# Kernel optimization log

Hardware: AMD Instinct MI355X
Metric: run time of the kernel (lower is better)

The kernel has to match this reference:

```python
import jax, jax.numpy as jnp
import numpy as np

B, D, E, H = 4, 128, 512, 512

def setup_inputs() -> dict:
    key = jax.random.key(0)
    k1, k2, k3, k4, k5 = jax.random.split(key, 5)
    s = 1.0 / np.sqrt(H)
    return {
        "x_decoder": jax.random.normal(k1, (B, D, H), dtype=jnp.float32),
        "x_encoder": jax.random.normal(k2, (B, E, H), dtype=jnp.float32),
        "mask": jnp.zeros((B, E), dtype=bool),
        "W1": jax.random.uniform(k3, (H, H), jnp.float32, -s, s),  # nn.Linear weight (out,in)
        "W2": jax.random.uniform(k4, (H, H), jnp.float32, -s, s),
        "v": jax.random.uniform(k5, (H,), jnp.float32, -s, s),     # Linear(H,1) weight squeezed
    }

def reference(x_decoder, x_encoder, mask, W1, W2, v):
    # w1(x_encoder): (B,E,H); w2(x_decoder): (B,D,H)
    enc_t = jnp.einsum('beh,oh->beo', x_encoder, W1)
    dec_t = jnp.einsum('bdh,oh->bdo', x_decoder, W2)
    # additive attention: tanh over broadcast sum (B,D,E,H), reduce with v -> (B,D,E)
    prod = jnp.einsum('bdeh,h->bde', jnp.tanh(dec_t[:, :, None, :] + enc_t[:, None, :, :]), v)
    prod = jnp.where(mask[:, None, :], -jnp.inf, prod)
    return jax.nn.log_softmax(prod, axis=-1)
```

## Files before the change

### kernel.cpp

```cpp
#include <hip/hip_runtime.h>
#include <math.h>

#define BATCH 4
#define DDIM  128
#define EDIM  512
#define HDIM  512

#define TANH_SCALE 2.8853900817779268f

typedef short short8v __attribute__((ext_vector_type(8)));
typedef float f32x4   __attribute__((ext_vector_type(4)));

#define EXP2F(x) __builtin_amdgcn_exp2f(x)
#define RCPF(x)  __builtin_amdgcn_rcpf(x)

static __device__ inline unsigned short f2bf(float f) {
    unsigned u = __float_as_uint(f);
    return (unsigned short)((u + 0x7FFFu + ((u >> 16) & 1u)) >> 16);
}
static __device__ inline unsigned pack_bf2(float f0, float f1) {
    unsigned u0 = __float_as_uint(f0), u1 = __float_as_uint(f1);
    u0 += 0x7FFFu + ((u0 >> 16) & 1u);
    u1 += 0x7FFFu + ((u1 >> 16) & 1u);
    return __builtin_amdgcn_perm(u1, u0, 0x07060302u);
}
static __device__ inline float bf2f(unsigned short h) {
    return __uint_as_float(((unsigned)h) << 16);
}

__global__ __launch_bounds__(256)
void gemm_both(const float* __restrict__ xdec, const float* __restrict__ W2,
               const float* __restrict__ xenc, const float* __restrict__ W1,
               unsigned short* __restrict__ P, unsigned short* __restrict__ Q) {
    __shared__ unsigned short As[2][64][40];
    __shared__ unsigned short Bs[2][64][40];

    const int id = blockIdx.x;
    const float *Ab, *Bb;
    unsigned short* Cb;
    int m0, n0;
    if (id < 64) {
        int b = id >> 4, r = id & 15;
        m0 = (r >> 3) * 64; n0 = (r & 7) * 64;
        Ab = xdec + (long)b * DDIM * HDIM;
        Bb = W2;
        Cb = P + (long)b * DDIM * HDIM;
    } else {
        int t2 = id - 64;
        int b = t2 >> 6, r = t2 & 63;
        m0 = (r >> 3) * 64; n0 = (r & 7) * 64;
        Ab = W1;
        Bb = xenc + (long)b * EDIM * HDIM;
        Cb = Q + (long)b * HDIM * EDIM;
    }

    const int t    = threadIdx.x;
    const int srow = t >> 2;
    const int skq  = (t & 3) << 3;

    const int wid = t >> 6, wm = wid >> 1, wn = wid & 1;
    const int l   = t & 63, lr = l & 15, c16 = l >> 4;

    f32x4 acc[2][2] = {};

    const float* ap = Ab + (long)(m0 + srow) * HDIM + skq;
    const float* bp = Bb + (long)(n0 + srow) * HDIM + skq;

    float4 a0 = *(const float4*)ap, a1 = *(const float4*)(ap + 4);
    float4 b0 = *(const float4*)bp, b1 = *(const float4*)(bp + 4);

    int cur = 0;
    for (int k0 = 0; k0 < HDIM; k0 += 32) {
        uint4 apk, bpk;
        apk.x = pack_bf2(a0.x, a0.y); apk.y = pack_bf2(a0.z, a0.w);
        apk.z = pack_bf2(a1.x, a1.y); apk.w = pack_bf2(a1.z, a1.w);
        bpk.x = pack_bf2(b0.x, b0.y); bpk.y = pack_bf2(b0.z, b0.w);
        bpk.z = pack_bf2(b1.x, b1.y); bpk.w = pack_bf2(b1.z, b1.w);
        *(uint4*)&As[cur][srow][skq] = apk;
        *(uint4*)&Bs[cur][srow][skq] = bpk;

        if (k0 + 32 < HDIM) {
            ap += 32; bp += 32;
            a0 = *(const float4*)ap; a1 = *(const float4*)(ap + 4);
            b0 = *(const float4*)bp; b1 = *(const float4*)(bp + 4);
        }

        asm volatile("s_waitcnt lgkmcnt(0)" ::: "memory");
        __builtin_amdgcn_s_barrier();
        __builtin_amdgcn_sched_barrier(0);

        short8v af[2], bf[2];
        #pragma unroll
        for (int fm = 0; fm < 2; ++fm)
            af[fm] = *(const short8v*)&As[cur][wm * 32 + fm * 16 + lr][c16 * 8];
        #pragma unroll
        for (int fn = 0; fn < 2; ++fn)
            bf[fn] = *(const short8v*)&Bs[cur][wn * 32 + fn * 16 + lr][c16 * 8];
        #pragma unroll
        for (int fm = 0; fm < 2; ++fm)
            #pragma unroll
            for (int fn = 0; fn < 2; ++fn)
                acc[fm][fn] = __builtin_amdgcn_mfma_f32_16x16x32_bf16(
                    af[fm], bf[fn], acc[fm][fn], 0, 0, 0);
        cur ^= 1;
    }

    const int crow = c16 << 2;
    #pragma unroll
    for (int fm = 0; fm < 2; ++fm)
        #pragma unroll
        for (int fn = 0; fn < 2; ++fn)
            #pragma unroll
            for (int r = 0; r < 4; ++r) {
                int rr = m0 + wm * 32 + fm * 16 + crow + r;
                int cc = n0 + wn * 32 + fn * 16 + lr;
                Cb[(long)rr * 512 + cc] = f2bf(EXP2F(TANH_SCALE * acc[fm][fn][r]));
            }
}

__global__ __launch_bounds__(512)
void attn_partial(const unsigned short* __restrict__ P,
                  const unsigned short* __restrict__ Q,
                  const float* __restrict__ vw,
                  float* __restrict__ partial) {
    const int g     = blockIdx.x;
    const int xcd   = g & 7;
    const int b     = xcd & 3;
    const int idx   = g >> 3;
    const int chunk = idx & 3;
    const int dp    = (idx >> 2) + ((xcd >> 2) << 5);
    const int pair  = b * 64 + dp;
    const int bd0   = pair * 2;
    const int t     = threadIdx.x;
    const int eq    = t & 127;
    const int hg    = t >> 7;
    const int h0    = chunk * 128;

    __shared__ float4 combo[128];
    __shared__ float  lds[4][128][8];

    if (t < 128) {
        int h = h0 + t;
        combo[t] = make_float4(bf2f(P[bd0 * HDIM + h]),
                               bf2f(P[(bd0 + 1) * HDIM + h]),
                               -2.0f * vw[h], 0.0f);
    }
    __syncthreads();

    const unsigned short* qb =
        Q + b * HDIM * EDIM + (h0 + hg * 32) * EDIM + eq * 4;
    float a00 = 0.f, a01 = 0.f, a02 = 0.f, a03 = 0.f;
    float a10 = 0.f, a11 = 0.f, a12 = 0.f, a13 = 0.f;
    #pragma unroll 8
    for (int ii = 0; ii < 32; ++ii) {
        uint2  qv = *(const uint2*)(qb + (size_t)ii * EDIM);
        float4 c  = combo[hg * 32 + ii];
        float q0 = __uint_as_float(qv.x << 16);
        float q1 = __uint_as_float(qv.x & 0xffff0000u);
        float q2 = __uint_as_float(qv.y << 16);
        float q3 = __uint_as_float(qv.y & 0xffff0000u);
        a00 = fmaf(c.z, RCPF(fmaf(c.x, q0, 1.0f)), a00);
        a01 = fmaf(c.z, RCPF(fmaf(c.x, q1, 1.0f)), a01);
        a02 = fmaf(c.z, RCPF(fmaf(c.x, q2, 1.0f)), a02);
        a03 = fmaf(c.z, RCPF(fmaf(c.x, q3, 1.0f)), a03);
        a10 = fmaf(c.z, RCPF(fmaf(c.y, q0, 1.0f)), a10);
        a11 = fmaf(c.z, RCPF(fmaf(c.y, q1, 1.0f)), a11);
        a12 = fmaf(c.z, RCPF(fmaf(c.y, q2, 1.0f)), a12);
        a13 = fmaf(c.z, RCPF(fmaf(c.y, q3, 1.0f)), a13);
    }

    float* myl = &lds[hg][eq][0];
    myl[0] = a00; myl[1] = a01; myl[2] = a02; myl[3] = a03;
    myl[4] = a10; myl[5] = a11; myl[6] = a12; myl[7] = a13;
    __syncthreads();

    float* pp = partial + ((size_t)pair * 4 + chunk) * 1024;
    #pragma unroll
    for (int rep = 0; rep < 2; ++rep) {
        int pos = t + rep * 512;
        int d = pos >> 9, e = pos & 511;
        int j = d * 4 + (e & 3), eqi = e >> 2;
        float v = (lds[0][eqi][j] + lds[1][eqi][j]) +
                  (lds[2][eqi][j] + lds[3][eqi][j]);
        pp[pos] = v;
    }
}

__global__ __launch_bounds__(512)
void lsm_final(const float* __restrict__ partial,
               const unsigned char* __restrict__ mask,
               float* __restrict__ out) {
    const int pair = blockIdx.x;
    const int b    = pair >> 6;
    const int bd0  = pair * 2;
    const int e    = threadIdx.x;

    __shared__ float red0[8], red1[8];

    const float* pp = partial + (size_t)pair * 4096;
    float acc0 = (pp[e]        + pp[1024 + e]) + (pp[2048 + e] + pp[3072 + e]);
    float acc1 = (pp[512 + e]  + pp[1536 + e]) + (pp[2560 + e] + pp[3584 + e]);

    const bool mk = mask[b * EDIM + e];
    float val0 = mk ? -INFINITY : acc0;
    float val1 = mk ? -INFINITY : acc1;

    const int wid = e >> 6, lid = e & 63;

    float m0 = val0, m1 = val1;
    #pragma unroll
    for (int o = 32; o >= 1; o >>= 1) {
        m0 = fmaxf(m0, __shfl_xor(m0, o));
        m1 = fmaxf(m1, __shfl_xor(m1, o));
    }
    if (lid == 0) { red0[wid] = m0; red1[wid] = m1; }
    __syncthreads();
    m0 = red0[0]; m1 = red1[0];
    #pragma unroll
    for (int i = 1; i < 8; ++i) { m0 = fmaxf(m0, red0[i]); m1 = fmaxf(m1, red1[i]); }
    __syncthreads();

    float s0 = __expf(val0 - m0), s1 = __expf(val1 - m1);
    #pragma unroll
    for (int o = 32; o >= 1; o >>= 1) {
        s0 += __shfl_xor(s0, o);
        s1 += __shfl_xor(s1, o);
    }
    if (lid == 0) { red0[wid] = s0; red1[wid] = s1; }
    __syncthreads();
    float tot0 = 0.f, tot1 = 0.f;
    #pragma unroll
    for (int i = 0; i < 8; ++i) { tot0 += red0[i]; tot1 += red1[i]; }

    out[(long)bd0 * EDIM + e]       = val0 - m0 - __logf(tot0);
    out[(long)(bd0 + 1) * EDIM + e] = val1 - m1 - __logf(tot1);
}

extern "C" void kernel_launch(void* const* d_in, const int* in_sizes, int n_in,
                              void* d_out, int out_size, void* d_ws, size_t ws_size,
                              hipStream_t stream) {
    const float*         xdec = (const float*)d_in[0];
    const float*         xenc = (const float*)d_in[1];
    const unsigned char* mask = (const unsigned char*)d_in[2];
    const float*         W1   = (const float*)d_in[3];
    const float*         W2   = (const float*)d_in[4];
    const float*         vw   = (const float*)d_in[5];
    float*               out  = (float*)d_out;

    unsigned short* P = (unsigned short*)d_ws;
    unsigned short* Q = P + 262144;
    float* partial    = (float*)(Q + 1048576);

    gemm_both<<<320, 256, 0, stream>>>(xdec, W2, xenc, W1, P, Q);
    attn_partial<<<1024, 512, 0, stream>>>(P, Q, vw, partial);
    lsm_final<<<256, 512, 0, stream>>>(partial, mask, out);
}
```

Measured before the change: 35.92 us.

## Combine pairs of reciprocal terms over a common denominator using packed FP32 math

Adds two adjacent h terms v0/x + v1/y by computing (v0*y + v1*x)/(x*y) with v_pk_fma/v_pk_mul inline asm. This halves the number of transcendental reciprocal instructions, replacing them with packed FMAs. The LDS combo layout is repacked into float2 pairs and the reduction buffer is padded to 9 to avoid bank conflicts. The risk is overflow or precision loss in the product denominator, and the inline asm ties the code to the gfx9 packed-FP32 instructions.

```diff
diff --git a/kernel.cpp b/kernel.cpp
--- a/kernel.cpp
+++ b/kernel.cpp
@@ -10,6 +10,7 @@
 
 typedef short short8v __attribute__((ext_vector_type(8)));
 typedef float f32x4   __attribute__((ext_vector_type(4)));
+typedef float f32x2   __attribute__((ext_vector_type(2)));
 
 #define EXP2F(x) __builtin_amdgcn_exp2f(x)
 #define RCPF(x)  __builtin_amdgcn_rcpf(x)
@@ -136,14 +137,16 @@
     const int hg    = t >> 7;
     const int h0    = chunk * 128;
 
-    __shared__ float4 combo[128];
-    __shared__ float  lds[4][128][8];
-
-    if (t < 128) {
-        int h = h0 + t;
-        combo[t] = make_float4(bf2f(P[bd0 * HDIM + h]),
-                               bf2f(P[(bd0 + 1) * HDIM + h]),
-                               -2.0f * vw[h], 0.0f);
+    __shared__ f32x2 combo2[64][3];
+    __shared__ float lds[4][128][9];
+
+    if (t < 64) {
+        int h = h0 + t * 2;
+        f32x2 p0, p1, vv;
+        p0.x = bf2f(P[bd0 * HDIM + h]);       p0.y = bf2f(P[bd0 * HDIM + h + 1]);
+        p1.x = bf2f(P[(bd0 + 1) * HDIM + h]); p1.y = bf2f(P[(bd0 + 1) * HDIM + h + 1]);
+        vv.x = -2.0f * vw[h];                 vv.y = -2.0f * vw[h + 1];
+        combo2[t][0] = p0; combo2[t][1] = p1; combo2[t][2] = vv;
     }
     __syncthreads();
 
@@ -151,23 +154,47 @@
         Q + b * HDIM * EDIM + (h0 + hg * 32) * EDIM + eq * 4;
     float a00 = 0.f, a01 = 0.f, a02 = 0.f, a03 = 0.f;
     float a10 = 0.f, a11 = 0.f, a12 = 0.f, a13 = 0.f;
-    #pragma unroll 8
-    for (int ii = 0; ii < 32; ++ii) {
-        uint2  qv = *(const uint2*)(qb + (size_t)ii * EDIM);
-        float4 c  = combo[hg * 32 + ii];
-        float q0 = __uint_as_float(qv.x << 16);
-        float q1 = __uint_as_float(qv.x & 0xffff0000u);
-        float q2 = __uint_as_float(qv.y << 16);
-        float q3 = __uint_as_float(qv.y & 0xffff0000u);
-        a00 = fmaf(c.z, RCPF(fmaf(c.x, q0, 1.0f)), a00);
-        a01 = fmaf(c.z, RCPF(fmaf(c.x, q1, 1.0f)), a01);
-        a02 = fmaf(c.z, RCPF(fmaf(c.x, q2, 1.0f)), a02);
-        a03 = fmaf(c.z, RCPF(fmaf(c.x, q3, 1.0f)), a03);
-        a10 = fmaf(c.z, RCPF(fmaf(c.y, q0, 1.0f)), a10);
-        a11 = fmaf(c.z, RCPF(fmaf(c.y, q1, 1.0f)), a11);
-        a12 = fmaf(c.z, RCPF(fmaf(c.y, q2, 1.0f)), a12);
-        a13 = fmaf(c.z, RCPF(fmaf(c.y, q3, 1.0f)), a13);
-    }
+    f32x2 ones; ones.x = 1.0f; ones.y = 1.0f;
+
+#define PAIR_SET(Pp, q0p, q1p, VV, accA, accB)                                  \
+    {                                                                           \
+        f32x2 xp, yp, den, tt, num;                                             \
+        asm("v_pk_fma_f32 %0, %1, %2, %3 op_sel_hi:[0,1,1]"                     \
+            : "=v"(xp) : "v"(Pp), "v"(q0p), "v"(ones));                         \
+        asm("v_pk_fma_f32 %0, %1, %2, %3 op_sel:[1,0,0] op_sel_hi:[1,1,1]"      \
+            : "=v"(yp) : "v"(Pp), "v"(q1p), "v"(ones));                         \
+        asm("v_pk_mul_f32 %0, %1, %2" : "=v"(den) : "v"(xp), "v"(yp));          \
+        asm("v_pk_mul_f32 %0, %1, %2 op_sel:[1,0] op_sel_hi:[1,1]"              \
+            : "=v"(tt) : "v"(VV), "v"(xp));                                     \
+        asm("v_pk_fma_f32 %0, %1, %2, %3 op_sel_hi:[0,1,1]"                     \
+            : "=v"(num) : "v"(VV), "v"(yp), "v"(tt));                           \
+        accA = fmaf(num.x, RCPF(den.x), accA);                                  \
+        accB = fmaf(num.y, RCPF(den.y), accB);                                  \
+    }
+
+    #pragma unroll 4
+    for (int ii = 0; ii < 16; ++ii) {
+        uint2 qv0 = *(const uint2*)(qb + (size_t)(2 * ii) * EDIM);
+        uint2 qv1 = *(const uint2*)(qb + (size_t)(2 * ii + 1) * EDIM);
+        f32x2 P0 = combo2[hg * 16 + ii][0];
+        f32x2 P1 = combo2[hg * 16 + ii][1];
+        f32x2 VV = combo2[hg * 16 + ii][2];
+        f32x2 qA0, qB0, qA1, qB1;
+        qA0.x = __uint_as_float(qv0.x << 16);
+        qA0.y = __uint_as_float(qv0.x & 0xffff0000u);
+        qB0.x = __uint_as_float(qv0.y << 16);
+        qB0.y = __uint_as_float(qv0.y & 0xffff0000u);
+        qA1.x = __uint_as_float(qv1.x << 16);
+        qA1.y = __uint_as_float(qv1.x & 0xffff0000u);
+        qB1.x = __uint_as_float(qv1.y << 16);
+        qB1.y = __uint_as_float(qv1.y & 0xffff0000u);
+
+        PAIR_SET(P0, qA0, qA1, VV, a00, a01);
+        PAIR_SET(P0, qB0, qB1, VV, a02, a03);
+        PAIR_SET(P1, qA0, qA1, VV, a10, a11);
+        PAIR_SET(P1, qB0, qB1, VV, a12, a13);
+    }
+#undef PAIR_SET
 
     float* myl = &lds[hg][eq][0];
     myl[0] = a00; myl[1] = a01; myl[2] = a02; myl[3] = a03;
@@ -176,8 +203,8 @@
 
     float* pp = partial + ((size_t)pair * 4 + chunk) * 1024;
     #pragma unroll
-    for (int rep = 0; rep < 2; ++rep) {
-        int pos = t + rep * 512;
+    for (int rp = 0; rp < 2; ++rp) {
+        int pos = t + rp * 512;
         int d = pos >> 9, e = pos & 511;
         int j = d * 4 + (e & 3), eqi = e >> 2;
         float v = (lds[0][eqi][j] + lds[1][eqi][j]) +
```

After: 33.77 us. 1.06x faster.
